# Performance work log

Hardware: AMD Instinct MI355X
Metric: run time of the kernel (lower is better)

## Reference

```python
import jax, jax.numpy as jnp
import numpy as np

B, C, M = 8192, 1024, 4096  # batch, controller width, memory_size


def setup_inputs() -> dict:
    key = jax.random.key(0)
    k1, k2, k3 = jax.random.split(key, 3)
    memory = jax.random.normal(k1, (B, M), dtype=jnp.float32)
    controller_output = jax.random.normal(k2, (B, C), dtype=jnp.float32)
    W = jax.random.normal(k3, (C, M), dtype=jnp.float32) * 0.02  # Dense kernel
    b = jnp.zeros((M,), dtype=jnp.float32)                       # Dense bias
    return {"memory": memory, "controller_output": controller_output, "W": W, "b": b}


def _l2_normalize(x, eps=1e-12):
    # matches tf.linalg.l2_normalize: x / sqrt(max(sum(x^2), eps))
    return x / jnp.sqrt(jnp.maximum(jnp.sum(x * x, axis=-1, keepdims=True), eps))


def reference(memory, controller_output, W, b):
    # Dense key projection followed by softmax over memory width
    key_vec = jax.nn.softmax(controller_output @ W + b, axis=-1)        # [B, M]
    # tf.keras.losses.cosine_similarity = -sum(l2n(a) * l2n(b), -1)
    sims = -jnp.sum(_l2_normalize(key_vec) * _l2_normalize(memory), axis=-1)  # [B]
    read_weights = jax.nn.softmax(sims, axis=-1)                        # softmax over B (as in source)
    read_vector = jnp.sum(read_weights[:, None] * memory, axis=1)       # [B]
    return read_vector
```

## Files before the change

kernel.cpp:

```cpp
#include <hip/hip_runtime.h>

#define NB 8192
#define NC 1024
#define NM 4096
#define NCH 16

typedef __attribute__((ext_vector_type(8))) short bf16x8;
typedef __attribute__((ext_vector_type(4))) float f32x4;

__device__ __forceinline__ unsigned short f2bf(float x) {
  unsigned int u = __float_as_uint(x);
  u += 0x7FFFu + ((u >> 16) & 1u);
  return (unsigned short)(u >> 16);
}
__device__ __forceinline__ unsigned int pk2(float a, float b) {
  return (unsigned int)f2bf(a) | ((unsigned int)f2bf(b) << 16);
}

__device__ __forceinline__ void gload_lds16(const void* g, void* l) {
  __builtin_amdgcn_global_load_lds(
      (const __attribute__((address_space(1))) unsigned int*)g,
      (__attribute__((address_space(3))) unsigned int*)l, 16, 0, 0);
}

#define DSR(dst, addr, IMM) \
  asm volatile("ds_read_b128 %0, %1 offset:" IMM : "=v"(dst) : "v"(addr))

__global__ __launch_bounds__(256) void convA_k(const float* __restrict__ src,
                                               unsigned short* __restrict__ dst) {
  const size_t i = ((size_t)blockIdx.x * 256 + threadIdx.x) * 8;
  const float4* s = reinterpret_cast<const float4*>(src + i);
  float4 x0 = s[0], x1 = s[1];
  int4 o = make_int4((int)pk2(x0.x, x0.y), (int)pk2(x0.z, x0.w),
                     (int)pk2(x1.x, x1.y), (int)pk2(x1.z, x1.w));
  *reinterpret_cast<int4*>(dst + i) = o;
}

__global__ __launch_bounds__(256) void convW_k(const float* __restrict__ W,
                                               unsigned short* __restrict__ Wt) {
  __shared__ float tile[64][65];
  const int n0 = blockIdx.x * 64, k0 = blockIdx.y * 64;
  const int t = threadIdx.x;
  const int r = t >> 2, q = t & 3;
  const float4* src = reinterpret_cast<const float4*>(W + (size_t)(k0 + r) * NM + n0 + q * 16);
  float4 x0 = src[0], x1 = src[1], x2 = src[2], x3 = src[3];
  float* tr = &tile[r][q * 16];
  tr[0]=x0.x; tr[1]=x0.y; tr[2]=x0.z;  tr[3]=x0.w;
  tr[4]=x1.x; tr[5]=x1.y; tr[6]=x1.z;  tr[7]=x1.w;
  tr[8]=x2.x; tr[9]=x2.y; tr[10]=x2.z; tr[11]=x2.w;
  tr[12]=x3.x; tr[13]=x3.y; tr[14]=x3.z; tr[15]=x3.w;
  __syncthreads();
  unsigned int pk[8];
#pragma unroll
  for (int i = 0; i < 8; ++i)
    pk[i] = pk2(tile[q * 16 + 2 * i][r], tile[q * 16 + 2 * i + 1][r]);
  int4* dst = reinterpret_cast<int4*>(Wt + (size_t)(n0 + r) * NC + k0 + q * 16);
  dst[0] = make_int4((int)pk[0], (int)pk[1], (int)pk[2], (int)pk[3]);
  dst[1] = make_int4((int)pk[4], (int)pk[5], (int)pk[6], (int)pk[7]);
}

__global__ __launch_bounds__(512) void gemm_fused(
    const unsigned short* __restrict__ Abf, const float* __restrict__ memry,
    const unsigned short* __restrict__ Wt, const float* __restrict__ bvec,
    float* __restrict__ pdotg, float* __restrict__ pesqg,
    float* __restrict__ pmsqg, float* __restrict__ pmsg) {
  __shared__ __align__(16) unsigned short LDS[2][4][8192];
  const int bm = blockIdx.x, bn = blockIdx.y;
  const int row0 = bm * 256, col0 = bn * 256;
  const int t = threadIdx.x;
  const int wid = t >> 6, lane = t & 63;
  const int wr = wid >> 2, wc = wid & 3;
  const int l15 = lane & 15, lg = lane >> 4;
  const int ga8 = (lg ^ ((l15 >> 1) & 3)) * 8;

  f32x4 acc[8][4];
#pragma unroll
  for (int mi = 0; mi < 8; ++mi)
#pragma unroll
    for (int ni = 0; ni < 4; ++ni) acc[mi][ni] = (f32x4){0.f, 0.f, 0.f, 0.f};

  const unsigned ldsbase =
      (unsigned)(uintptr_t)(__attribute__((address_space(3))) void*)&LDS[0][0][0];
  const unsigned abase = ldsbase + ((wr * 128 + l15) * 32 + ga8) * 2;
  const unsigned bbase = ldsbase + 32768 + ((wc * 64 + l15) * 32 + ga8) * 2;

  const int srow0 = t >> 2;
  const int sk8 = ((t & 3) ^ ((srow0 >> 1) & 3)) * 8;
  const unsigned short* gA = Abf + (size_t)(row0 + srow0) * NC + sk8;
  const unsigned short* gB = Wt + (size_t)(col0 + srow0) * NC + sk8;

#define STG(SL, TY, KT)                                                      \
  {                                                                          \
    const unsigned short* s0 = ((TY) <= 1 ? gA : gB) + (KT) * 64 + ((TY)&1) * 32; \
    gload_lds16(s0, &LDS[SL][TY][t * 8]);                                    \
    gload_lds16(s0 + (size_t)128 * NC, &LDS[SL][TY][t * 8 + 4096]);          \
  }
#define NOSTG
#define VM6 asm volatile("s_waitcnt vmcnt(6)" ::: "memory")
#define VM0 asm volatile("s_waitcnt vmcnt(0)" ::: "memory")
#define NOVM

#define PH(SL, S, MH, RDB, STAGE, VM)                                        \
  {                                                                          \
    if (RDB) {                                                               \
      const unsigned ba = bbase + (SL)*65536 + (S)*16384;                    \
      DSR(b[0], ba, "0");    DSR(b[1], ba, "1024");                          \
      DSR(b[2], ba, "2048"); DSR(b[3], ba, "3072");                          \
    }                                                                        \
    const unsigned aa = abase + (SL)*65536 + (S)*16384 + (MH)*4096;          \
    DSR(a[0], aa, "0");    DSR(a[1], aa, "1024");                            \
    DSR(a[2], aa, "2048"); DSR(a[3], aa, "3072");                            \
    STAGE;                                                                   \
    VM;                                                                      \
    __builtin_amdgcn_s_barrier();                                            \
    asm volatile("s_waitcnt lgkmcnt(0)" ::: "memory");                       \
    __builtin_amdgcn_sched_barrier(0);                                       \
    __builtin_amdgcn_s_setprio(1);                                           \
    _Pragma("unroll") for (int mi = 0; mi < 4; ++mi)                         \
        _Pragma("unroll") for (int ni = 0; ni < 4; ++ni)                     \
            acc[(MH)*4 + mi][ni] = __builtin_amdgcn_mfma_f32_16x16x32_bf16(  \
                a[mi], b[ni], acc[(MH)*4 + mi][ni], 0, 0, 0);                \
    __builtin_amdgcn_s_setprio(0);                                           \
    __builtin_amdgcn_s_barrier();                                            \
    __builtin_amdgcn_sched_barrier(0);                                       \
  }

  STG(0, 2, 0); STG(0, 0, 0); STG(0, 3, 0); STG(0, 1, 0);
  STG(1, 2, 1); STG(1, 0, 1); STG(1, 3, 1);
  VM6;
  __builtin_amdgcn_s_barrier();
  __builtin_amdgcn_sched_barrier(0);

  bf16x8 a[4], b[4];
  for (int it = 0; it < 7; ++it) {
    const int c1 = 2 * it + 1, c2 = 2 * it + 2, c3 = 2 * it + 3;
    PH(0, 0, 0, true,  STG(1, 1, c1), NOVM);
    PH(0, 0, 1, false, STG(0, 2, c2), NOVM);
    PH(0, 1, 0, true,  STG(0, 0, c2), NOVM);
    PH(0, 1, 1, false, STG(0, 3, c2), VM6);
    PH(1, 0, 0, true,  STG(0, 1, c2), NOVM);
    PH(1, 0, 1, false, STG(1, 2, c3), NOVM);
    PH(1, 1, 0, true,  STG(1, 0, c3), NOVM);
    PH(1, 1, 1, false, STG(1, 3, c3), VM6);
  }
  PH(0, 0, 0, true,  STG(1, 1, 15), NOVM);
  PH(0, 0, 1, false, NOSTG, NOVM);
  PH(0, 1, 0, true,  NOSTG, NOVM);
  PH(0, 1, 1, false, NOSTG, VM0);
  PH(1, 0, 0, true,  NOSTG, NOVM);
  PH(1, 0, 1, false, NOSTG, NOVM);
  PH(1, 1, 0, true,  NOSTG, NOVM);
  PH(1, 1, 1, false, NOSTG, NOVM);
#undef PH
#undef STG

  unsigned short (*e_lds)[256] = reinterpret_cast<unsigned short(*)[256]>(&LDS[0][0][0]);
  float bv[4];
#pragma unroll
  for (int ni = 0; ni < 4; ++ni) bv[ni] = bvec[col0 + wc * 64 + ni * 16 + l15];
#pragma unroll
  for (int mi = 0; mi < 8; ++mi)
#pragma unroll
    for (int ni = 0; ni < 4; ++ni)
#pragma unroll
      for (int j = 0; j < 4; ++j) {
        const int rl = wr * 128 + mi * 16 + 4 * lg + j;
        const int cl = wc * 64 + ni * 16 + l15;
        e_lds[rl][cl] = f2bf(__expf(acc[mi][ni][j] + bv[ni]));
      }
  __syncthreads();

  {
    const int halfl = lane >> 5, l31 = lane & 31;
    const int rbase = wid * 32;
#pragma unroll 4
    for (int i = 0; i < 16; ++i) {
      const int rl = rbase + 2 * i + halfl;
      const float4* mp = reinterpret_cast<const float4*>(
          memry + (size_t)(row0 + rl) * NM + col0 + l31 * 8);
      float4 m0 = mp[0], m1 = mp[1];
      bf16x8 ev = *reinterpret_cast<const bf16x8*>(&e_lds[rl][l31 * 8]);
      float mv[8] = {m0.x, m0.y, m0.z, m0.w, m1.x, m1.y, m1.z, m1.w};
      float pd = 0.f, pe = 0.f, pq = 0.f, pm = 0.f;
#pragma unroll
      for (int k = 0; k < 8; ++k) {
        float e = __uint_as_float(((unsigned int)(unsigned short)ev[k]) << 16);
        pd += e * mv[k]; pe += e * e; pq += mv[k] * mv[k]; pm += mv[k];
      }
#pragma unroll
      for (int s = 1; s < 32; s <<= 1) {
        pd += __shfl_xor(pd, s); pe += __shfl_xor(pe, s);
        pq += __shfl_xor(pq, s); pm += __shfl_xor(pm, s);
      }
      if (l31 == 0) {
        const int idx = (row0 + rl) * NCH + bn;
        pdotg[idx] = pd; pesqg[idx] = pe; pmsqg[idx] = pq; pmsg[idx] = pm;
      }
    }
  }
}

__global__ __launch_bounds__(256) void finalize_k(
    const float* __restrict__ pd, const float* __restrict__ pe,
    const float* __restrict__ pq, const float* __restrict__ pm,
    float* __restrict__ sims, float* __restrict__ mst) {
  const int r = blockIdx.x * 256 + threadIdx.x;
  float d = 0.f, e = 0.f, q = 0.f, m = 0.f;
#pragma unroll
  for (int i = 0; i < NCH; ++i) {
    d += pd[r * NCH + i];
    e += pe[r * NCH + i];
    q += pq[r * NCH + i];
    m += pm[r * NCH + i];
  }
  sims[r] = -d / (sqrtf(fmaxf(e, 1e-12f)) * sqrtf(fmaxf(q, 1e-12f)));
  mst[r] = m;
}

__global__ __launch_bounds__(1024) void softmax_out_k(
    const float* __restrict__ sims, const float* __restrict__ mst,
    float* __restrict__ out) {
  __shared__ float red[16];
  const int t = threadIdx.x;
  float v[8];
  float mx = -1e30f;
#pragma unroll
  for (int i = 0; i < 8; ++i) {
    v[i] = sims[t + i * 1024];
    mx = fmaxf(mx, v[i]);
  }
#pragma unroll
  for (int s = 1; s < 64; s <<= 1) mx = fmaxf(mx, __shfl_xor(mx, s));
  if ((t & 63) == 0) red[t >> 6] = mx;
  __syncthreads();
  float m2 = red[0];
#pragma unroll
  for (int i = 1; i < 16; ++i) m2 = fmaxf(m2, red[i]);
  mx = m2;
  float sum = 0.f;
#pragma unroll
  for (int i = 0; i < 8; ++i) sum += __expf(v[i] - mx);
#pragma unroll
  for (int s = 1; s < 64; s <<= 1) sum += __shfl_xor(sum, s);
  __syncthreads();
  if ((t & 63) == 0) red[t >> 6] = sum;
  __syncthreads();
  float s2 = 0.f;
#pragma unroll
  for (int i = 0; i < 16; ++i) s2 += red[i];
  const float inv = 1.0f / s2;
#pragma unroll
  for (int i = 0; i < 8; ++i)
    out[t + i * 1024] = __expf(v[i] - mx) * inv * mst[t + i * 1024];
}

extern "C" void kernel_launch(void* const* d_in, const int* in_sizes, int n_in,
                              void* d_out, int out_size, void* d_ws, size_t ws_size,
                              hipStream_t stream) {
  const float* memry = (const float*)d_in[0];
  const float* co    = (const float*)d_in[1];
  const float* W     = (const float*)d_in[2];
  const float* bvec  = (const float*)d_in[3];
  float* out = (float*)d_out;

  char* w = (char*)d_ws;
  unsigned short* Wt  = (unsigned short*)w;
  unsigned short* Abf = Wt + (size_t)NM * NC;
  float* pdot = (float*)(Abf + (size_t)NB * NC);
  float* pesq = pdot + (size_t)NB * NCH;
  float* pmsq = pesq + (size_t)NB * NCH;
  float* pms  = pmsq + (size_t)NB * NCH;
  float* sims = pms  + (size_t)NB * NCH;
  float* mst  = sims + NB;

  convA_k<<<(size_t)NB * NC / (256 * 8), 256, 0, stream>>>(co, Abf);
  convW_k<<<dim3(NM / 64, NC / 64), 256, 0, stream>>>(W, Wt);
  gemm_fused<<<dim3(NB / 256, NM / 256), 512, 0, stream>>>(Abf, memry, Wt, bvec,
                                                           pdot, pesq, pmsq, pms);
  finalize_k<<<NB / 256, 256, 0, stream>>>(pdot, pesq, pmsq, pms, sims, mst);
  softmax_out_k<<<1, 1024, 0, stream>>>(sims, mst, out);
}
```

Measured before the change: 109.1 us.

## Merge conversion kernels, remap GEMM tiles, prefetch memory, swizzle epilogue LDS

Combines the two bf16 conversion kernels into one launch to save a kernel launch and the gap between them. Remaps GEMM block indices so blocks scheduled together spread across XCDs. Issues loads of the memory tile during the final MFMA phases to warm the cache ahead of the epilogue. Also XOR-swizzles the epilogue LDS layout to reduce bank conflicts and unrolls the reduction loop further. These are several unrelated tweaks that add register pressure and code complexity.

```diff
diff --git a/kernel.cpp b/kernel.cpp
--- a/kernel.cpp
+++ b/kernel.cpp
@@ -26,37 +26,39 @@
 #define DSR(dst, addr, IMM) \
   asm volatile("ds_read_b128 %0, %1 offset:" IMM : "=v"(dst) : "v"(addr))
 
-__global__ __launch_bounds__(256) void convA_k(const float* __restrict__ src,
-                                               unsigned short* __restrict__ dst) {
-  const size_t i = ((size_t)blockIdx.x * 256 + threadIdx.x) * 8;
-  const float4* s = reinterpret_cast<const float4*>(src + i);
-  float4 x0 = s[0], x1 = s[1];
-  int4 o = make_int4((int)pk2(x0.x, x0.y), (int)pk2(x0.z, x0.w),
-                     (int)pk2(x1.x, x1.y), (int)pk2(x1.z, x1.w));
-  *reinterpret_cast<int4*>(dst + i) = o;
-}
-
-__global__ __launch_bounds__(256) void convW_k(const float* __restrict__ W,
-                                               unsigned short* __restrict__ Wt) {
+__global__ __launch_bounds__(256) void prep_k(const float* __restrict__ W,
+                                              unsigned short* __restrict__ Wt,
+                                              const float* __restrict__ coin,
+                                              unsigned short* __restrict__ Abf) {
   __shared__ float tile[64][65];
-  const int n0 = blockIdx.x * 64, k0 = blockIdx.y * 64;
+  const int bid = blockIdx.x;
   const int t = threadIdx.x;
-  const int r = t >> 2, q = t & 3;
-  const float4* src = reinterpret_cast<const float4*>(W + (size_t)(k0 + r) * NM + n0 + q * 16);
-  float4 x0 = src[0], x1 = src[1], x2 = src[2], x3 = src[3];
-  float* tr = &tile[r][q * 16];
-  tr[0]=x0.x; tr[1]=x0.y; tr[2]=x0.z;  tr[3]=x0.w;
-  tr[4]=x1.x; tr[5]=x1.y; tr[6]=x1.z;  tr[7]=x1.w;
-  tr[8]=x2.x; tr[9]=x2.y; tr[10]=x2.z; tr[11]=x2.w;
-  tr[12]=x3.x; tr[13]=x3.y; tr[14]=x3.z; tr[15]=x3.w;
-  __syncthreads();
-  unsigned int pk[8];
-#pragma unroll
-  for (int i = 0; i < 8; ++i)
-    pk[i] = pk2(tile[q * 16 + 2 * i][r], tile[q * 16 + 2 * i + 1][r]);
-  int4* dst = reinterpret_cast<int4*>(Wt + (size_t)(n0 + r) * NC + k0 + q * 16);
-  dst[0] = make_int4((int)pk[0], (int)pk[1], (int)pk[2], (int)pk[3]);
-  dst[1] = make_int4((int)pk[4], (int)pk[5], (int)pk[6], (int)pk[7]);
+  if (bid < 1024) {
+    const int n0 = (bid & 63) * 64, k0 = (bid >> 6) * 64;
+    const int r = t >> 2, q = t & 3;
+    const float4* src = reinterpret_cast<const float4*>(W + (size_t)(k0 + r) * NM + n0 + q * 16);
+    float4 x0 = src[0], x1 = src[1], x2 = src[2], x3 = src[3];
+    float* tr = &tile[r][q * 16];
+    tr[0]=x0.x; tr[1]=x0.y; tr[2]=x0.z;  tr[3]=x0.w;
+    tr[4]=x1.x; tr[5]=x1.y; tr[6]=x1.z;  tr[7]=x1.w;
+    tr[8]=x2.x; tr[9]=x2.y; tr[10]=x2.z; tr[11]=x2.w;
+    tr[12]=x3.x; tr[13]=x3.y; tr[14]=x3.z; tr[15]=x3.w;
+    __syncthreads();
+    unsigned int pk[8];
+#pragma unroll
+    for (int i = 0; i < 8; ++i)
+      pk[i] = pk2(tile[q * 16 + 2 * i][r], tile[q * 16 + 2 * i + 1][r]);
+    int4* dst = reinterpret_cast<int4*>(Wt + (size_t)(n0 + r) * NC + k0 + q * 16);
+    dst[0] = make_int4((int)pk[0], (int)pk[1], (int)pk[2], (int)pk[3]);
+    dst[1] = make_int4((int)pk[4], (int)pk[5], (int)pk[6], (int)pk[7]);
+  } else {
+    const size_t i = ((size_t)(bid - 1024) * 256 + t) * 8;
+    const float4* s = reinterpret_cast<const float4*>(coin + i);
+    float4 x0 = s[0], x1 = s[1];
+    int4 o = make_int4((int)pk2(x0.x, x0.y), (int)pk2(x0.z, x0.w),
+                       (int)pk2(x1.x, x1.y), (int)pk2(x1.z, x1.w));
+    *reinterpret_cast<int4*>(Abf + i) = o;
+  }
 }
 
 __global__ __launch_bounds__(512) void gemm_fused(
@@ -65,7 +67,9 @@
     float* __restrict__ pdotg, float* __restrict__ pesqg,
     float* __restrict__ pmsqg, float* __restrict__ pmsg) {
   __shared__ __align__(16) unsigned short LDS[2][4][8192];
-  const int bm = blockIdx.x, bn = blockIdx.y;
+  const int didx = blockIdx.y * 32 + blockIdx.x;
+  const int nl = (didx & 7) * 64 + (didx >> 3);
+  const int bm = nl & 31, bn = nl >> 5;
   const int row0 = bm * 256, col0 = bn * 256;
   const int t = threadIdx.x;
   const int wid = t >> 6, lane = t & 63;
@@ -94,6 +98,12 @@
     const unsigned short* s0 = ((TY) <= 1 ? gA : gB) + (KT) * 64 + ((TY)&1) * 32; \
     gload_lds16(s0, &LDS[SL][TY][t * 8]);                                    \
     gload_lds16(s0 + (size_t)128 * NC, &LDS[SL][TY][t * 8 + 4096]);          \
+  }
+#define PREF(i)                                                              \
+  {                                                                          \
+    const int c = t + (i)*512;                                               \
+    float pv = memry[(size_t)(row0 + (c >> 3)) * NM + col0 + (c & 7) * 32];  \
+    asm volatile("" ::"v"(pv));                                              \
   }
 #define NOSTG
 #define VM6 asm volatile("s_waitcnt vmcnt(6)" ::: "memory")
@@ -147,12 +157,13 @@
   PH(0, 0, 1, false, NOSTG, NOVM);
   PH(0, 1, 0, true,  NOSTG, NOVM);
   PH(0, 1, 1, false, NOSTG, VM0);
-  PH(1, 0, 0, true,  NOSTG, NOVM);
-  PH(1, 0, 1, false, NOSTG, NOVM);
-  PH(1, 1, 0, true,  NOSTG, NOVM);
-  PH(1, 1, 1, false, NOSTG, NOVM);
+  PH(1, 0, 0, true,  PREF(0), NOVM);
+  PH(1, 0, 1, false, PREF(1), NOVM);
+  PH(1, 1, 0, true,  PREF(2), NOVM);
+  PH(1, 1, 1, false, PREF(3), NOVM);
 #undef PH
 #undef STG
+#undef PREF
 
   unsigned short (*e_lds)[256] = reinterpret_cast<unsigned short(*)[256]>(&LDS[0][0][0]);
   float bv[4];
@@ -166,20 +177,21 @@
       for (int j = 0; j < 4; ++j) {
         const int rl = wr * 128 + mi * 16 + 4 * lg + j;
         const int cl = wc * 64 + ni * 16 + l15;
-        e_lds[rl][cl] = f2bf(__expf(acc[mi][ni][j] + bv[ni]));
+        e_lds[rl][cl ^ (((rl >> 2) & 3) << 4)] = f2bf(__expf(acc[mi][ni][j] + bv[ni]));
       }
   __syncthreads();
 
   {
     const int halfl = lane >> 5, l31 = lane & 31;
     const int rbase = wid * 32;
-#pragma unroll 4
+#pragma unroll 8
     for (int i = 0; i < 16; ++i) {
       const int rl = rbase + 2 * i + halfl;
       const float4* mp = reinterpret_cast<const float4*>(
           memry + (size_t)(row0 + rl) * NM + col0 + l31 * 8);
       float4 m0 = mp[0], m1 = mp[1];
-      bf16x8 ev = *reinterpret_cast<const bf16x8*>(&e_lds[rl][l31 * 8]);
+      bf16x8 ev = *reinterpret_cast<const bf16x8*>(
+          &e_lds[rl][(l31 * 8) ^ (((rl >> 2) & 3) << 4)]);
       float mv[8] = {m0.x, m0.y, m0.z, m0.w, m1.x, m1.y, m1.z, m1.w};
       float pd = 0.f, pe = 0.f, pq = 0.f, pm = 0.f;
 #pragma unroll
@@ -273,8 +285,7 @@
   float* sims = pms  + (size_t)NB * NCH;
   float* mst  = sims + NB;
 
-  convA_k<<<(size_t)NB * NC / (256 * 8), 256, 0, stream>>>(co, Abf);
-  convW_k<<<dim3(NM / 64, NC / 64), 256, 0, stream>>>(W, Wt);
+  prep_k<<<1024 + (size_t)NB * NC / (256 * 8), 256, 0, stream>>>(W, Wt, co, Abf);
   gemm_fused<<<dim3(NB / 256, NM / 256), 512, 0, stream>>>(Abf, memry, Wt, bvec,
                                                            pdot, pesq, pmsq, pms);
   finalize_k<<<NB / 256, 256, 0, stream>>>(pdot, pesq, pmsq, pms, sims, mst);
```

New measurement: 132.9 us. 21.8% more time.
